# Kernel optimization log

Hardware: AMD Instinct MI355X
Metric: run time of the kernel (lower is better)

## Reference

```python
import jax, jax.numpy as jnp
import numpy as np

N = 100000      # nodes
E = 1600000     # graph edges
P = 100000      # pos/neg candidate edges
D_IN = 128
D_H = 128
ALPHA = 0.1
NUM_LAYERS = 3


def _linear_params(key, d_in, d_out):
    k1, k2 = jax.random.split(key)
    s = 1.0 / np.sqrt(d_in)
    W = jax.random.uniform(k1, (d_in, d_out), minval=-s, maxval=s, dtype=jnp.float32)
    b = jax.random.uniform(k2, (d_out,), minval=-s, maxval=s, dtype=jnp.float32)
    return W, b


def setup_inputs() -> dict:
    key = jax.random.key(0)
    ks = jax.random.split(key, 12)
    x = jax.random.normal(ks[0], (N, D_IN), dtype=jnp.float32)
    src = jax.random.randint(ks[1], (E,), 0, N)
    dst = jax.random.randint(ks[2], (E,), 0, N)
    pos_src = jax.random.randint(ks[3], (P,), 0, N)
    pos_dst = jax.random.randint(ks[4], (P,), 0, N)
    neg_src = jax.random.randint(ks[5], (P,), 0, N)
    neg_dst = jax.random.randint(ks[6], (P,), 0, N)
    lin1_w, lin1_b = _linear_params(ks[7], D_IN, D_H)
    lin2_w, lin2_b = _linear_params(ks[8], D_H, D_H)
    p1_w, p1_b = _linear_params(ks[9], D_H, D_H)
    p2_w, p2_b = _linear_params(ks[10], D_H, D_H)
    p3_w, p3_b = _linear_params(ks[11], D_H, 1)
    # GPR gamma coefficients: alpha*(1-alpha)^k, last = (1-alpha)^L
    gamma = ALPHA * (1.0 - ALPHA) ** np.arange(NUM_LAYERS + 1, dtype=np.float32)
    gamma[-1] = (1.0 - ALPHA) ** NUM_LAYERS
    gamma = jnp.asarray(gamma, dtype=jnp.float32)
    return {
        "x": x, "lin1_w": lin1_w, "lin1_b": lin1_b, "lin2_w": lin2_w, "lin2_b": lin2_b,
        "gamma": gamma, "p1_w": p1_w, "p1_b": p1_b, "p2_w": p2_w, "p2_b": p2_b,
        "p3_w": p3_w, "p3_b": p3_b,
        "src": src, "dst": dst,
        "pos_src": pos_src, "pos_dst": pos_dst, "neg_src": neg_src, "neg_dst": neg_dst,
    }


def _graph_conv(h, src, dst, n):
    # DGL GraphConv(weight=False, bias=False), norm='both':
    # out = D_in^{-1/2} A (D_out^{-1/2} h), degrees clamped to >= 1
    ones = jnp.ones(src.shape[0], dtype=h.dtype)
    deg_out = jnp.clip(jax.ops.segment_sum(ones, src, num_segments=n), 1.0)
    deg_in = jnp.clip(jax.ops.segment_sum(ones, dst, num_segments=n), 1.0)
    h = h * jax.lax.rsqrt(deg_out)[:, None]
    agg = jax.ops.segment_sum(h[src], dst, num_segments=n)  # [N, D]
    return agg * jax.lax.rsqrt(deg_in)[:, None]


def _predictor(e, p1_w, p1_b, p2_w, p2_b, p3_w, p3_b):
    e = jax.nn.relu(e @ p1_w + p1_b)
    e = jax.nn.relu(e @ p2_w + p2_b)
    return e @ p3_w + p3_b  # [P, 1]


def reference(x, lin1_w, lin1_b, lin2_w, lin2_b, gamma, p1_w, p1_b, p2_w, p2_b,
              p3_w, p3_b, src, dst, pos_src, pos_dst, neg_src, neg_dst):
    n = x.shape[0]
    h = jax.nn.relu(x @ lin1_w + lin1_b)
    h = h @ lin2_w + lin2_b
    rep = gamma[0] * h
    for l in range(NUM_LAYERS):
        h = _graph_conv(h, src, dst, n)
        rep = rep + gamma[l + 1] * h  # full-graph blocks: dstnodes == all nodes
    h = rep
    h_pos = _predictor(h[pos_src] * h[pos_dst], p1_w, p1_b, p2_w, p2_b, p3_w, p3_b)
    h_neg = _predictor(h[neg_src] * h[neg_dst], p1_w, p1_b, p2_w, p2_b, p3_w, p3_b)
    return (h_pos, h_neg)
```

## Files before the change

kernel.cpp:

```cpp
#include <hip/hip_runtime.h>

#define D 128

typedef _Float16 half8 __attribute__((ext_vector_type(8)));
typedef _Float16 f16x2 __attribute__((ext_vector_type(2)));
typedef float floatx4 __attribute__((ext_vector_type(4)));

static inline int cdiv(int a, int b){ return (a + b - 1) / b; }


__global__ __launch_bounds__(256) void zero_cnt_kernel(int* __restrict__ cnt_out,
                                                       int* __restrict__ cnt_in, int n)
{
    int i = blockIdx.x * 256 + threadIdx.x;
    if (i < n) { cnt_out[i] = 0; cnt_in[i] = 0; }
}

__global__ __launch_bounds__(256) void count_kernel(const int* __restrict__ src,
                                                    const int* __restrict__ dst,
                                                    int* __restrict__ cnt_out,
                                                    int* __restrict__ cnt_in, int E)
{
    int i = blockIdx.x * 256 + threadIdx.x;
    if (i < E) {
        atomicAdd(&cnt_out[src[i]], 1);
        atomicAdd(&cnt_in[dst[i]], 1);
    }
}

__global__ __launch_bounds__(256) void dinv_kernel(const int* __restrict__ cnt_out,
                                                   const int* __restrict__ cnt_in,
                                                   float* __restrict__ dinv_out,
                                                   float* __restrict__ dinv_in, int n)
{
    int i = blockIdx.x * 256 + threadIdx.x;
    if (i < n) {
        dinv_out[i] = rsqrtf(fmaxf((float)cnt_out[i], 1.0f));
        dinv_in[i]  = rsqrtf(fmaxf((float)cnt_in[i],  1.0f));
    }
}

__global__ __launch_bounds__(256) void scan_partial(const int* __restrict__ cnt,
                                                    int* __restrict__ pre,
                                                    int* __restrict__ blk_sums, int n)
{
    __shared__ int lds[256];
    int t = threadIdx.x;
    int base = blockIdx.x * 1024 + t * 4;
    int v0 = 0, v1 = 0, v2 = 0, v3 = 0;
    if (base + 0 < n) v0 = cnt[base + 0];
    if (base + 1 < n) v1 = cnt[base + 1];
    if (base + 2 < n) v2 = cnt[base + 2];
    if (base + 3 < n) v3 = cnt[base + 3];
    int ts = v0 + v1 + v2 + v3;
    lds[t] = ts;
    __syncthreads();
    for (int off = 1; off < 256; off <<= 1) {
        int add = (t >= off) ? lds[t - off] : 0;
        __syncthreads();
        lds[t] += add;
        __syncthreads();
    }
    int excl = lds[t] - ts;
    if (base + 0 < n) pre[base + 0] = excl;
    if (base + 1 < n) pre[base + 1] = excl + v0;
    if (base + 2 < n) pre[base + 2] = excl + v0 + v1;
    if (base + 3 < n) pre[base + 3] = excl + v0 + v1 + v2;
    if (t == 255) blk_sums[blockIdx.x] = lds[255];
}

__global__ void scan_blk(const int* __restrict__ blk_sums, int* __restrict__ blk_off, int nblk)
{
    if (threadIdx.x == 0 && blockIdx.x == 0) {
        int run = 0;
        for (int j = 0; j < nblk; ++j) { blk_off[j] = run; run += blk_sums[j]; }
    }
}

__global__ __launch_bounds__(256) void scan_final(const int* __restrict__ pre,
                                                  const int* __restrict__ blk_off,
                                                  int* __restrict__ row_start,
                                                  int* __restrict__ fill_ptr, int n, int E)
{
    int i = blockIdx.x * 256 + threadIdx.x;
    if (i < n) {
        int v = pre[i] + blk_off[i >> 10];
        row_start[i] = v;
        fill_ptr[i]  = v;
    }
    if (i == 0) row_start[n] = E;
}

__global__ __launch_bounds__(256) void fill_kernel(const int* __restrict__ src,
                                                   const int* __restrict__ dst,
                                                   int* __restrict__ fill_ptr,
                                                   int* __restrict__ esrc, int E)
{
    int i = blockIdx.x * 256 + threadIdx.x;
    if (i < E) {
        int p = atomicAdd(&fill_ptr[dst[i]], 1);
        esrc[p] = src[i];
    }
}

__global__ __launch_bounds__(256) void wt_kernel(const float* __restrict__ W,
                                                 _Float16* __restrict__ Wt)
{
    __shared__ float tile[32][33];
    const int b = blockIdx.x;
    const int tx = b & 3, ty = b >> 2;
    const int t = threadIdx.x;
    const int r = t >> 3, c4 = (t & 7) * 4;
    const float4 v = *(const float4*)&W[(size_t)(ty * 32 + r) * D + tx * 32 + c4];
    tile[r][c4 + 0] = v.x; tile[r][c4 + 1] = v.y;
    tile[r][c4 + 2] = v.z; tile[r][c4 + 3] = v.w;
    __syncthreads();
    _Float16* dst = Wt + (size_t)(tx * 32 + r) * D + ty * 32 + c4;
    dst[0] = (_Float16)tile[c4 + 0][r];
    dst[1] = (_Float16)tile[c4 + 1][r];
    dst[2] = (_Float16)tile[c4 + 2][r];
    dst[3] = (_Float16)tile[c4 + 3][r];
}

__global__ __launch_bounds__(256, 4) void conv_f16(const _Float16* __restrict__ hin,
                                                   _Float16* __restrict__ hout,
                                                   float* __restrict__ rep,
                                                   const int* __restrict__ row_start,
                                                   const int* __restrict__ esrc,
                                                   const float* __restrict__ dinv_out,
                                                   const float* __restrict__ dinv_in,
                                                   const float* __restrict__ gamma,
                                                   int lidx, int n)
{
    const int node = (blockIdx.x * 256 + threadIdx.x) >> 4;
    const int sub  = threadIdx.x & 15;
    if (node >= n) return;
    const int rs = row_start[node];
    const int re = row_start[node + 1];
    const half8* hb = (const half8*)hin;

    float acc[8] = {0.f, 0.f, 0.f, 0.f, 0.f, 0.f, 0.f, 0.f};
    int i = rs;
    for (; i + 1 < re; i += 2) {
        const int s0 = esrc[i];
        const int s1 = esrc[i + 1];
        const float c0 = dinv_out[s0];
        const float c1 = dinv_out[s1];
        const half8 v0 = hb[(size_t)s0 * 16 + sub];
        const half8 v1 = hb[(size_t)s1 * 16 + sub];
        #pragma unroll
        for (int j = 0; j < 8; ++j)
            acc[j] += (float)v0[j] * c0 + (float)v1[j] * c1;
    }
    if (i < re) {
        const int s0 = esrc[i];
        const float c0 = dinv_out[s0];
        const half8 v0 = hb[(size_t)s0 * 16 + sub];
        #pragma unroll
        for (int j = 0; j < 8; ++j)
            acc[j] += (float)v0[j] * c0;
    }

    const float di = dinv_in[node];
    const float g  = gamma[lidx];
    half8 o;
    #pragma unroll
    for (int j = 0; j < 8; ++j) {
        acc[j] *= di;
        o[j] = (_Float16)acc[j];
    }
    ((half8*)hout)[(size_t)node * 16 + sub] = o;

    floatx4* rp = (floatx4*)(rep + (size_t)node * D + sub * 8);
    floatx4 r0 = rp[0], r1 = rp[1];
    r0[0] += g * acc[0]; r0[1] += g * acc[1]; r0[2] += g * acc[2]; r0[3] += g * acc[3];
    r1[0] += g * acc[4]; r1[1] += g * acc[5]; r1[2] += g * acc[6]; r1[3] += g * acc[7];
    rp[0] = r0; rp[1] = r1;
}

__device__ __forceinline__ int lds_off(int r, int chunk)
{
    return r * D + ((chunk ^ (r & 15)) << 3);
}

template<int MODE>
__global__ __launch_bounds__(256, 2) void gemm_mfma(const float* __restrict__ Xf,
                                                    const _Float16* __restrict__ Xh,
                                                    const _Float16* __restrict__ Wt,
                                                    const float* __restrict__ B, int R,
                                                    _Float16* __restrict__ outh,
                                                    float* __restrict__ rep,
                                                    const float* __restrict__ gamma,
                                                    const int* __restrict__ ia,
                                                    const int* __restrict__ ib,
                                                    const float* __restrict__ w3,
                                                    const float* __restrict__ b3,
                                                    float* __restrict__ outsc)
{
    __shared__ _Float16 Als[D * D];
    __shared__ _Float16 Wls[D * D];
    const int t = threadIdx.x;
    const int rowbase = blockIdx.x * D;

    #pragma unroll
    for (int it = 0; it < 8; ++it) {
        const int r = it * 16 + (t >> 4);
        const int c = t & 15;
        *(half8*)&Wls[lds_off(r, c)] = *(const half8*)(Wt + (size_t)r * D + c * 8);
        int g = rowbase + r; if (g > R - 1) g = R - 1;
        half8 hv;
        if (MODE == 0) {
            const float4* ap = (const float4*)(Xf + (size_t)g * D + c * 8);
            float4 a0 = ap[0], a1 = ap[1];
            hv[0] = (_Float16)a0.x; hv[1] = (_Float16)a0.y;
            hv[2] = (_Float16)a0.z; hv[3] = (_Float16)a0.w;
            hv[4] = (_Float16)a1.x; hv[5] = (_Float16)a1.y;
            hv[6] = (_Float16)a1.z; hv[7] = (_Float16)a1.w;
        } else if (MODE == 2) {
            const float4* pa = (const float4*)(Xf + (size_t)ia[g] * D + c * 8);
            const float4* pb = (const float4*)(Xf + (size_t)ib[g] * D + c * 8);
            float4 a0 = pa[0], a1 = pa[1], b0 = pb[0], b1 = pb[1];
            hv[0] = (_Float16)(a0.x * b0.x); hv[1] = (_Float16)(a0.y * b0.y);
            hv[2] = (_Float16)(a0.z * b0.z); hv[3] = (_Float16)(a0.w * b0.w);
            hv[4] = (_Float16)(a1.x * b1.x); hv[5] = (_Float16)(a1.y * b1.y);
            hv[6] = (_Float16)(a1.z * b1.z); hv[7] = (_Float16)(a1.w * b1.w);
        } else {
            hv = *(const half8*)(Xh + (size_t)g * D + c * 8);
        }
        *(half8*)&Als[lds_off(r, c)] = hv;
    }
    __syncthreads();

    const int wid = t >> 6;
    const int l   = t & 63;
    const int lr  = l & 15;
    const int lq  = l >> 4;

    floatx4 acc[2][8];
    #pragma unroll
    for (int m = 0; m < 2; ++m)
        #pragma unroll
        for (int n = 0; n < 8; ++n) {
            acc[m][n][0] = 0.f; acc[m][n][1] = 0.f;
            acc[m][n][2] = 0.f; acc[m][n][3] = 0.f;
        }

    #pragma unroll
    for (int kk = 0; kk < 4; ++kk) {
        const int cc = kk * 4 + lq;
        half8 af[2], bf[8];
        #pragma unroll
        for (int m = 0; m < 2; ++m) {
            const int r = wid * 32 + m * 16 + lr;
            af[m] = *(half8*)&Als[lds_off(r, cc)];
        }
        #pragma unroll
        for (int n = 0; n < 8; ++n) {
            const int r = n * 16 + lr;
            bf[n] = *(half8*)&Wls[lds_off(r, cc)];
        }
        #pragma unroll
        for (int m = 0; m < 2; ++m)
            #pragma unroll
            for (int n = 0; n < 8; ++n)
                acc[m][n] = __builtin_amdgcn_mfma_f32_16x16x32_f16(af[m], bf[n], acc[m][n], 0, 0, 0);
    }

    if (MODE == 3) {
        float bv[8], wv[8];
        #pragma unroll
        for (int n = 0; n < 8; ++n) { bv[n] = B[n * 16 + lr]; wv[n] = w3[n * 16 + lr]; }
        const float bb = b3[0];
        #pragma unroll
        for (int m = 0; m < 2; ++m) {
            #pragma unroll
            for (int q = 0; q < 4; ++q) {
                float s = 0.f;
                #pragma unroll
                for (int n = 0; n < 8; ++n)
                    s += fmaxf(acc[m][n][q] + bv[n], 0.f) * wv[n];
                s += __shfl_xor(s, 1); s += __shfl_xor(s, 2);
                s += __shfl_xor(s, 4); s += __shfl_xor(s, 8);
                const int r = rowbase + wid * 32 + m * 16 + lq * 4 + q;
                if (lr == 0 && r < R) outsc[r] = s + bb;
            }
        }
    } else {
        float bv[8];
        #pragma unroll
        for (int n = 0; n < 8; ++n) bv[n] = B[n * 16 + lr];
        const float g0 = (MODE == 1) ? gamma[0] : 0.f;
        #pragma unroll
        for (int m = 0; m < 2; ++m) {
            #pragma unroll
            for (int q = 0; q < 4; ++q) {
                const int r = rowbase + wid * 32 + m * 16 + lq * 4 + q;
                if (r < R) {
                    #pragma unroll
                    for (int n = 0; n < 8; ++n) {
                        float v = acc[m][n][q] + bv[n];
                        if (MODE != 1) v = fmaxf(v, 0.f);
                        outh[(size_t)r * D + n * 16 + lr] = (_Float16)v;
                        if (MODE == 1) rep[(size_t)r * D + n * 16 + lr] = g0 * v;
                    }
                }
            }
        }
    }
}


extern "C" void kernel_launch(void* const* d_in, const int* in_sizes, int n_in,
                              void* d_out, int out_size, void* d_ws, size_t ws_size,
                              hipStream_t stream)
{
    const float* x      = (const float*)d_in[0];
    const float* lin1_w = (const float*)d_in[1];
    const float* lin1_b = (const float*)d_in[2];
    const float* lin2_w = (const float*)d_in[3];
    const float* lin2_b = (const float*)d_in[4];
    const float* gamma  = (const float*)d_in[5];
    const float* p1_w   = (const float*)d_in[6];
    const float* p1_b   = (const float*)d_in[7];
    const float* p2_w   = (const float*)d_in[8];
    const float* p2_b   = (const float*)d_in[9];
    const float* p3_w   = (const float*)d_in[10];
    const float* p3_b   = (const float*)d_in[11];
    const int* src     = (const int*)d_in[12];
    const int* dst     = (const int*)d_in[13];
    const int* pos_src = (const int*)d_in[14];
    const int* pos_dst = (const int*)d_in[15];
    const int* neg_src = (const int*)d_in[16];
    const int* neg_dst = (const int*)d_in[17];

    const int N = in_sizes[0] / D;
    const int E = in_sizes[12];
    const int P = in_sizes[14];

    char* base = (char*)d_ws;
    _Float16* bufB = (_Float16*)base;
    _Float16* bufA = bufB + (size_t)N * D;
    float*    rep  = (float*)(bufA + (size_t)N * D);
    _Float16* wt1  = (_Float16*)(rep + (size_t)N * D);
    _Float16* wt2  = wt1 + D * D;
    _Float16* wtp1 = wt2 + D * D;
    _Float16* wtp2 = wtp1 + D * D;
    char* ip = (char*)(wtp2 + D * D);
    int* cnt_out   = (int*)ip;  ip += (size_t)N * 4;
    int* cnt_in    = (int*)ip;  ip += (size_t)N * 4;
    int* pre       = (int*)ip;  ip += (size_t)N * 4;
    int* row_start = (int*)ip;  ip += (size_t)(N + 1) * 4;
    int* fill_ptr  = (int*)ip;  ip += (size_t)N * 4;
    int* blk_sums  = (int*)ip;  ip += 4096 * 4;
    int* blk_off   = (int*)ip;  ip += 4096 * 4;
    float* dinv_out = (float*)ip; ip += (size_t)N * 4;
    float* dinv_in  = (float*)ip; ip += (size_t)N * 4;
    int* esrc      = (int*)ip;  ip += (size_t)E * 4;
    _Float16* e1;
    if ((size_t)(2 * P) <= 2 * (size_t)N) {
        e1 = (_Float16*)base;
    } else {
        e1 = (_Float16*)ip; ip += (size_t)(2 * P) * D * 2;
    }

    zero_cnt_kernel<<<cdiv(N, 256), 256, 0, stream>>>(cnt_out, cnt_in, N);
    count_kernel<<<cdiv(E, 256), 256, 0, stream>>>(src, dst, cnt_out, cnt_in, E);
    dinv_kernel<<<cdiv(N, 256), 256, 0, stream>>>(cnt_out, cnt_in, dinv_out, dinv_in, N);
    int nblk = cdiv(N, 1024);
    scan_partial<<<nblk, 256, 0, stream>>>(cnt_in, pre, blk_sums, N);
    scan_blk<<<1, 64, 0, stream>>>(blk_sums, blk_off, nblk);
    scan_final<<<cdiv(N, 256), 256, 0, stream>>>(pre, blk_off, row_start, fill_ptr, N, E);
    fill_kernel<<<cdiv(E, 256), 256, 0, stream>>>(src, dst, fill_ptr, esrc, E);

    wt_kernel<<<16, 256, 0, stream>>>(lin1_w, wt1);
    wt_kernel<<<16, 256, 0, stream>>>(lin2_w, wt2);
    wt_kernel<<<16, 256, 0, stream>>>(p1_w, wtp1);
    wt_kernel<<<16, 256, 0, stream>>>(p2_w, wtp2);

    gemm_mfma<0><<<cdiv(N, 128), 256, 0, stream>>>(x, nullptr, wt1, lin1_b, N,
        bufB, nullptr, nullptr, nullptr, nullptr, nullptr, nullptr, nullptr);
    gemm_mfma<1><<<cdiv(N, 128), 256, 0, stream>>>(nullptr, bufB, wt2, lin2_b, N,
        bufA, rep, gamma, nullptr, nullptr, nullptr, nullptr, nullptr);

    conv_f16<<<cdiv(N * 16, 256), 256, 0, stream>>>(bufA, bufB, rep, row_start, esrc,
                                                    dinv_out, dinv_in, gamma, 1, N);
    conv_f16<<<cdiv(N * 16, 256), 256, 0, stream>>>(bufB, bufA, rep, row_start, esrc,
                                                    dinv_out, dinv_in, gamma, 2, N);
    conv_f16<<<cdiv(N * 16, 256), 256, 0, stream>>>(bufA, bufB, rep, row_start, esrc,
                                                    dinv_out, dinv_in, gamma, 3, N);

    gemm_mfma<2><<<cdiv(P, 128), 256, 0, stream>>>(rep, nullptr, wtp1, p1_b, P,
        e1, nullptr, nullptr, pos_src, pos_dst, nullptr, nullptr, nullptr);
    gemm_mfma<2><<<cdiv(P, 128), 256, 0, stream>>>(rep, nullptr, wtp1, p1_b, P,
        e1 + (size_t)P * D, nullptr, nullptr, neg_src, neg_dst, nullptr, nullptr, nullptr);
    gemm_mfma<3><<<cdiv(2 * P, 128), 256, 0, stream>>>(nullptr, e1, wtp2, p2_b, 2 * P,
        nullptr, nullptr, nullptr, nullptr, nullptr, p3_w, p3_b, (float*)d_out);
}
```

Baseline: 697.8 us.

## Replace global-atomic degree counting with LDS-privatized partitioned histograms

Degree counting previously did two global atomics per edge. It now uses per-block LDS histograms over 16384-bin node ranges and edge chunks, writes partial histograms, then reduces them in a separate kernel that also computes the inverse-sqrt degrees and in-counts. This removes contended global atomics and folds the zero and dinv kernels into the new pipeline. The cost is that each block reads its whole edge chunk once per node range (about 7x redundant reads of src and dst), plus extra workspace and partial-histogram traffic.

```diff
diff --git a/kernel.cpp b/kernel.cpp
--- a/kernel.cpp
+++ b/kernel.cpp
@@ -1,44 +1,68 @@
 #include <hip/hip_runtime.h>
 
 #define D 128
+#define HBINS 16384
+#define HCHUNKS 32
 
 typedef _Float16 half8 __attribute__((ext_vector_type(8)));
-typedef _Float16 f16x2 __attribute__((ext_vector_type(2)));
 typedef float floatx4 __attribute__((ext_vector_type(4)));
 
-static inline int cdiv(int a, int b){ return (a + b - 1) / b; }
-
-
-__global__ __launch_bounds__(256) void zero_cnt_kernel(int* __restrict__ cnt_out,
-                                                       int* __restrict__ cnt_in, int n)
-{
-    int i = blockIdx.x * 256 + threadIdx.x;
-    if (i < n) { cnt_out[i] = 0; cnt_in[i] = 0; }
-}
-
-__global__ __launch_bounds__(256) void count_kernel(const int* __restrict__ src,
-                                                    const int* __restrict__ dst,
-                                                    int* __restrict__ cnt_out,
-                                                    int* __restrict__ cnt_in, int E)
-{
-    int i = blockIdx.x * 256 + threadIdx.x;
-    if (i < E) {
-        atomicAdd(&cnt_out[src[i]], 1);
-        atomicAdd(&cnt_in[dst[i]], 1);
-    }
-}
-
-__global__ __launch_bounds__(256) void dinv_kernel(const int* __restrict__ cnt_out,
-                                                   const int* __restrict__ cnt_in,
+__host__ __device__ static inline int cdiv(int a, int b){ return (a + b - 1) / b; }
+
+__global__ __launch_bounds__(256) void hist_kernel(const int* __restrict__ vals, int E,
+                                                   int* __restrict__ part)
+{
+    __shared__ int h[HBINS];
+    const int r = blockIdx.x / HCHUNKS;
+    const int c = blockIdx.x % HCHUNKS;
+    for (int i = threadIdx.x; i < HBINS; i += 256) h[i] = 0;
+    __syncthreads();
+
+    int elen = cdiv(E, HCHUNKS);
+    elen = (elen + 3) & ~3;
+    const int lo = c * elen;
+    const int hi = min(E, lo + elen);
+    if (lo < hi) {
+        const int nfull = (hi - lo) >> 2;
+        const int4* v4 = (const int4*)(vals + lo);
+        for (int i = threadIdx.x; i < nfull; i += 256) {
+            const int4 v = v4[i];
+            if ((v.x >> 14) == r) atomicAdd(&h[v.x & (HBINS - 1)], 1);
+            if ((v.y >> 14) == r) atomicAdd(&h[v.y & (HBINS - 1)], 1);
+            if ((v.z >> 14) == r) atomicAdd(&h[v.z & (HBINS - 1)], 1);
+            if ((v.w >> 14) == r) atomicAdd(&h[v.w & (HBINS - 1)], 1);
+        }
+        for (int i = lo + (nfull << 2) + threadIdx.x; i < hi; i += 256) {
+            const int v = vals[i];
+            if ((v >> 14) == r) atomicAdd(&h[v & (HBINS - 1)], 1);
+        }
+    }
+    __syncthreads();
+    int* dstp = part + (size_t)blockIdx.x * HBINS;
+    for (int i = threadIdx.x; i < HBINS; i += 256) dstp[i] = h[i];
+}
+
+__global__ __launch_bounds__(256) void hist_reduce(const int* __restrict__ partA,
+                                                   const int* __restrict__ partB,
+                                                   int* __restrict__ cnt_in,
                                                    float* __restrict__ dinv_out,
                                                    float* __restrict__ dinv_in, int n)
 {
-    int i = blockIdx.x * 256 + threadIdx.x;
-    if (i < n) {
-        dinv_out[i] = rsqrtf(fmaxf((float)cnt_out[i], 1.0f));
-        dinv_in[i]  = rsqrtf(fmaxf((float)cnt_in[i],  1.0f));
-    }
-}
+    const int i = blockIdx.x * 256 + threadIdx.x;
+    if (i >= n) return;
+    const int r = i >> 14, b = i & (HBINS - 1);
+    const size_t base = ((size_t)r * HCHUNKS) * HBINS + b;
+    int so = 0, si = 0;
+    #pragma unroll
+    for (int c = 0; c < HCHUNKS; ++c) {
+        so += partA[base + (size_t)c * HBINS];
+        si += partB[base + (size_t)c * HBINS];
+    }
+    dinv_out[i] = rsqrtf(fmaxf((float)so, 1.0f));
+    dinv_in[i]  = rsqrtf(fmaxf((float)si, 1.0f));
+    cnt_in[i] = si;
+}
+
 
 __global__ __launch_bounds__(256) void scan_partial(const int* __restrict__ cnt,
                                                     int* __restrict__ pre,
@@ -336,6 +360,7 @@
     const int N = in_sizes[0] / D;
     const int E = in_sizes[12];
     const int P = in_sizes[14];
+    const int NR = cdiv(N, HBINS);
 
     char* base = (char*)d_ws;
     _Float16* bufB = (_Float16*)base;
@@ -346,7 +371,6 @@
     _Float16* wtp1 = wt2 + D * D;
     _Float16* wtp2 = wtp1 + D * D;
     char* ip = (char*)(wtp2 + D * D);
-    int* cnt_out   = (int*)ip;  ip += (size_t)N * 4;
     int* cnt_in    = (int*)ip;  ip += (size_t)N * 4;
     int* pre       = (int*)ip;  ip += (size_t)N * 4;
     int* row_start = (int*)ip;  ip += (size_t)(N + 1) * 4;
@@ -356,6 +380,8 @@
     float* dinv_out = (float*)ip; ip += (size_t)N * 4;
     float* dinv_in  = (float*)ip; ip += (size_t)N * 4;
     int* esrc      = (int*)ip;  ip += (size_t)E * 4;
+    int* partA     = (int*)ip;  ip += (size_t)NR * HCHUNKS * HBINS * 4;
+    int* partB     = (int*)ip;  ip += (size_t)NR * HCHUNKS * HBINS * 4;
     _Float16* e1;
     if ((size_t)(2 * P) <= 2 * (size_t)N) {
         e1 = (_Float16*)base;
@@ -363,9 +389,10 @@
         e1 = (_Float16*)ip; ip += (size_t)(2 * P) * D * 2;
     }
 
-    zero_cnt_kernel<<<cdiv(N, 256), 256, 0, stream>>>(cnt_out, cnt_in, N);
-    count_kernel<<<cdiv(E, 256), 256, 0, stream>>>(src, dst, cnt_out, cnt_in, E);
-    dinv_kernel<<<cdiv(N, 256), 256, 0, stream>>>(cnt_out, cnt_in, dinv_out, dinv_in, N);
+    hist_kernel<<<NR * HCHUNKS, 256, 0, stream>>>(src, E, partA);
+    hist_kernel<<<NR * HCHUNKS, 256, 0, stream>>>(dst, E, partB);
+    hist_reduce<<<cdiv(N, 256), 256, 0, stream>>>(partA, partB, cnt_in,
+                                                  dinv_out, dinv_in, N);
     int nblk = cdiv(N, 1024);
     scan_partial<<<nblk, 256, 0, stream>>>(cnt_in, pre, blk_sums, N);
     scan_blk<<<1, 64, 0, stream>>>(blk_sums, blk_off, nblk);
```

Result: faster. 642.2 us (-8.0%).
